# Kernel optimization log

Measured on AMD Instinct MI355X. Metric: run time of the kernel, lower is better.

The kernel has to match this reference:

```python
import jax, jax.numpy as jnp
import numpy as np
import math

NUM_HEADS = 8
KEY_DIM = 32
VALUE_DIM = 32
ERF = 3                      # local window (erf x erf), N = 1 + ERF*ERF key/query positions
PAD = (ERF - 1) // 2
STRIDE = 2
OUT_CH = 256


def unfold_2d(x, k, p, s):
    """Mirror of F.unfold -> (B, k*k, C, Ho, Wo), window index row-major (kh, kw)."""
    B, C, H, W = x.shape
    xp = jnp.pad(x, ((0, 0), (0, 0), (p, p), (p, p)))
    Ho = (H + 2 * p - k) // s + 1
    Wo = (W + 2 * p - k) // s + 1
    pats = [xp[:, :, i:i + s * (Ho - 1) + 1:s, j:j + s * (Wo - 1) + 1:s]
            for i in range(k) for j in range(k)]
    return jnp.stack(pats, axis=1)


def fold_2d(pats, out_hw, k, p, s):
    """Mirror of F.fold (overlap-add inverse of unfold_2d)."""
    B, kk, C, Ho, Wo = pats.shape
    H, W = out_hw
    out = jnp.zeros((B, C, H + 2 * p, W + 2 * p), pats.dtype)
    idx = 0
    for i in range(k):
        for j in range(k):
            out = out.at[:, :, i:i + s * (Ho - 1) + 1:s, j:j + s * (Wo - 1) + 1:s].add(pats[:, idx])
            idx += 1
    return out[:, :, p:p + H, p:p + W]


def setup_inputs() -> dict:
    key = jax.random.key(0)
    ks = jax.random.split(key, 10)
    B = 2
    d = {
        "top_feat": jax.random.normal(ks[0], (B, OUT_CH, 64, 64), jnp.float32),
        "bot_feat": jax.random.normal(ks[1], (B, OUT_CH, 128, 128), jnp.float32),
    }
    qkv_names = ["W_top_key", "W_top_query", "W_top_value", "W_bot_key", "W_bot_query", "W_bot_value"]
    for n, kk in zip(qkv_names, ks[2:8]):
        out_dim = NUM_HEADS * (KEY_DIM if ("key" in n or "query" in n) else VALUE_DIM)
        d[n] = 0.01 * jax.random.normal(kk, (out_dim, OUT_CH), jnp.float32)  # 1x1 conv, no bias
    d["W_top_fuse"] = 0.01 * jax.random.normal(ks[8], (OUT_CH, NUM_HEADS * VALUE_DIM), jnp.float32)
    d["W_bot_fuse"] = 0.01 * jax.random.normal(ks[9], (OUT_CH, NUM_HEADS * VALUE_DIM), jnp.float32)
    return d


def _forward(top_feat, bot_feat, W_top_key, W_top_query, W_top_value,
             W_bot_key, W_bot_query, W_bot_value, W_top_fuse, W_bot_fuse):
    B, _, H, W = top_feat.shape
    Hb, Wb = bot_feat.shape[2], bot_feat.shape[3]

    def proj(x, Wm, dim):  # 1x1 conv then split heads -> (B, h, dim, H', W')
        y = jnp.einsum('oc,bchw->bohw', Wm, x)
        return y.reshape(B, NUM_HEADS, dim, x.shape[2], x.shape[3])

    def unfold_heads(x):  # (B, h, d, Hb, Wb) -> (B, h, e*e, d, H, W)
        d = x.shape[2]
        u = unfold_2d(x.reshape(B * NUM_HEADS, d, Hb, Wb), ERF, PAD, STRIDE)
        return u.reshape(B, NUM_HEADS, ERF * ERF, d, u.shape[3], u.shape[4])

    tK = proj(top_feat, W_top_key, KEY_DIM)[:, :, None]      # (B, h, 1, kd, H, W)
    tQ = proj(top_feat, W_top_query, KEY_DIM)[:, :, None]
    tV = proj(top_feat, W_top_value, VALUE_DIM)[:, :, None]
    bK = unfold_heads(proj(bot_feat, W_bot_key, KEY_DIM))    # (B, h, e*e, kd, H, W)
    bQ = unfold_heads(proj(bot_feat, W_bot_query, KEY_DIM))
    bV = unfold_heads(proj(bot_feat, W_bot_value, VALUE_DIM))

    key_ = jnp.concatenate([tK, bK], axis=2)   # (B, h, N, kd, H, W), N = 1 + e*e
    query = jnp.concatenate([tQ, bQ], axis=2)
    value = jnp.concatenate([tV, bV], axis=2)

    # weight[b,n,k,q,h,w] = <key_k, query_q> / sqrt(kd)   (NOTE: no softmax in original)
    weight = jnp.einsum('bnkdhw,bnqdhw->bnkqhw', key_, query) / math.sqrt(KEY_DIM)
    # out[b,n,q,v,h,w] = sum_k weight[...] * value_k
    out = jnp.einsum('bnkqhw,bnkvhw->bnqvhw', weight, value)  # (B, h, N, vd, H, W)

    top_ret = out[:, :, 0].reshape(B, NUM_HEADS * VALUE_DIM, H, W)
    bot_pat = out[:, :, 1:].reshape(B * NUM_HEADS, ERF * ERF, VALUE_DIM, H, W)
    bot_ret = fold_2d(bot_pat, (Hb, Wb), ERF, PAD, STRIDE).reshape(B, NUM_HEADS * VALUE_DIM, Hb, Wb)

    top_out = jnp.einsum('oc,bchw->bohw', W_top_fuse, top_ret)
    bot_out = jnp.einsum('oc,bchw->bohw', W_bot_fuse, bot_ret)
    return top_out, bot_out


def reference(top_feat, bot_feat, W_top_key, W_top_query, W_top_value,
              W_bot_key, W_bot_query, W_bot_value, W_top_fuse, W_bot_fuse):
    return _forward(top_feat, bot_feat, W_top_key, W_top_query, W_top_value,
                    W_bot_key, W_bot_query, W_bot_value, W_top_fuse, W_bot_fuse)
```

## Files before the change

### kernel.cpp

```cpp
#include <hip/hip_runtime.h>
#include <hip/hip_bf16.h>
#include <math.h>


typedef __attribute__((ext_vector_type(8))) short  bh8;
typedef __attribute__((ext_vector_type(4))) short  bh4;
typedef __attribute__((ext_vector_type(4))) float  f32x4;
typedef unsigned short u16;

static __device__ __forceinline__ u16 f2b(float x) {
    __hip_bfloat16 h = __float2bfloat16(x);
    return __builtin_bit_cast(u16, h);
}
static __device__ __forceinline__ float b2f(u16 u) {
    unsigned v = ((unsigned)u) << 16;
    return __builtin_bit_cast(float, v);
}

static __device__ __forceinline__ void gload16(const u16* g, u16* l) {
    __builtin_amdgcn_global_load_lds(
        (const __attribute__((address_space(1))) unsigned int*)g,
        (__attribute__((address_space(3))) unsigned int*)l, 16, 0, 0);
}

__global__ __launch_bounds__(256) void k_cvt_w(
    const float* w0, const float* w1, const float* w2, const float* w3,
    const float* w4, const float* w5, const float* w6, const float* w7,
    u16* __restrict__ Wb)
{
    const float* srcs[8] = {w0,w1,w2,w3,w4,w5,w6,w7};
    const float* src = srcs[blockIdx.y];
    int i = (blockIdx.x * 256 + threadIdx.x) * 4;
    float4 v = *(const float4*)&src[i];
    u16 tmp[4] = { f2b(v.x), f2b(v.y), f2b(v.z), f2b(v.w) };
    *(uint2*)&Wb[(size_t)blockIdx.y * 65536 + i] = *(uint2*)tmp;
}

__global__ __launch_bounds__(512) void k_proj(
    const float* __restrict__ top_feat, const float* __restrict__ bot_feat,
    const u16* __restrict__ Wb,
    u16* __restrict__ tK, u16* __restrict__ bK, size_t TOPU, size_t BOTU)
{
    const int lbid  = (blockIdx.x & 7) * 120 + (blockIdx.x >> 3);
    const int yb    = lbid / 3;
    const int n0    = (lbid - yb * 3) * 256;
    const bool istop = yb < 64;
    const float* feat = istop ? top_feat : bot_feat;
    const u16* Bw   = istop ? Wb : (Wb + 3 * 65536);
    u16* Yp         = istop ? tK : bK;
    const size_t arrsz = istop ? TOPU : BOTU;
    const int S     = istop ? 4096 : 16384;
    const int m0g   = (istop ? yb : (yb - 64)) * 128;
    const int b     = istop ? (m0g >> 12) : (m0g >> 14);
    const int pix0  = m0g & (S - 1);
    const float* Xb = feat + (size_t)b * 256 * S;
    const int t  = threadIdx.x;
    const int w  = t >> 6, wl = t & 63, l16 = wl & 15, grp = wl >> 4;
    const int wm = w >> 2, wn = w & 3;
    const int apix = t & 127;
    const int oct  = t >> 7;

    __shared__ __align__(16) u16 AT[2][128 * 32];
    __shared__ __align__(16) u16 BT[2][256 * 32];

    float rA[8];

#define PA_LOAD(kk) do {                                                      \
        _Pragma("unroll")                                                     \
        for (int e = 0; e < 8; ++e)                                           \
            rA[e] = Xb[(size_t)((kk) + oct * 8 + e) * S + pix0 + apix];       \
    } while (0)

#define PA_WRITE(bufi) do {                                                   \
        u16 tmp[8];                                                           \
        _Pragma("unroll")                                                     \
        for (int e = 0; e < 8; ++e) tmp[e] = f2b(rA[e]);                      \
        int slot = oct ^ ((apix >> 1) & 3);                                   \
        *(uint4*)&AT[bufi][apix * 32 + slot * 8] = *(uint4*)tmp;              \
    } while (0)

#define PB_STAGE(bufi, kk) do {                                               \
        _Pragma("unroll")                                                     \
        for (int it = 0; it < 2; ++it) {                                      \
            int lin = it * 512 + t;                                           \
            int row = lin >> 2, c = lin & 3;                                  \
            int cs = c ^ ((row >> 1) & 3);                                    \
            gload16(&Bw[(size_t)(n0 + row) * 256 + (kk) + cs * 8],            \
                    &BT[bufi][lin * 8]);                                      \
        }                                                                     \
    } while (0)

    f32x4 acc[4][4];
    #pragma unroll
    for (int i = 0; i < 4; ++i)
        #pragma unroll
        for (int j = 0; j < 4; ++j) acc[i][j] = (f32x4){0.f, 0.f, 0.f, 0.f};

    PA_LOAD(0);
    PB_STAGE(0, 0);
    PA_WRITE(0);
    int cur = 0;
    for (int kt = 0; kt < 8; ++kt) {
        __syncthreads();
        if (kt < 7) {
            PA_LOAD((kt + 1) * 32);
            PB_STAGE(cur ^ 1, (kt + 1) * 32);
        }
        bh8 af[4], bf[4];
        #pragma unroll
        for (int mi = 0; mi < 4; ++mi) {
            int row = wm * 64 + mi * 16 + l16;
            int slot = grp ^ ((row >> 1) & 3);
            af[mi] = *(const bh8*)&AT[cur][row * 32 + slot * 8];
        }
        #pragma unroll
        for (int ni = 0; ni < 4; ++ni) {
            int row = wn * 64 + ni * 16 + l16;
            int slot = grp ^ ((row >> 1) & 3);
            bf[ni] = *(const bh8*)&BT[cur][row * 32 + slot * 8];
        }
        #pragma unroll
        for (int mi = 0; mi < 4; ++mi)
            #pragma unroll
            for (int ni = 0; ni < 4; ++ni)
                acc[mi][ni] = __builtin_amdgcn_mfma_f32_16x16x32_bf16(
                    af[mi], bf[ni], acc[mi][ni], 0, 0, 0);
        if (kt < 7) PA_WRITE(cur ^ 1);
        cur ^= 1;
    }
#undef PA_LOAD
#undef PA_WRITE
#undef PB_STAGE

    #pragma unroll
    for (int mi = 0; mi < 4; ++mi)
        #pragma unroll
        for (int ni = 0; ni < 4; ++ni)
            #pragma unroll
            for (int r = 0; r < 4; ++r) {
                int m = m0g + wm*64 + mi*16 + grp*4 + r;
                int n = n0 + wn*64 + ni*16 + l16;
                Yp[(size_t)(n >> 8) * arrsz + (size_t)m * 256 + (n & 255)]
                    = f2b(acc[mi][ni][r]);
            }
}

#define GEMM_STAGE(bufi, kk) do {                                             \
        _Pragma("unroll")                                                     \
        for (int it = 0; it < 2; ++it) {                                      \
            int lin = it * 256 + t;                                           \
            int row = lin >> 3, c = lin & 7;                                  \
            int cs = c ^ (row & 7);                                           \
            gload16(&A[(size_t)(m0 + row) * 256 + (kk) + cs * 8],             \
                    &AT[bufi][lin * 8]);                                      \
        }                                                                     \
        _Pragma("unroll")                                                     \
        for (int it = 0; it < 8; ++it) {                                      \
            int lin = it * 256 + t;                                           \
            int row = lin >> 3, c = lin & 7;                                  \
            int cs = c ^ (row & 7);                                           \
            gload16(&B[(size_t)(n0 + row) * 256 + (kk) + cs * 8],             \
                    &BT[bufi][lin * 8]);                                      \
        }                                                                     \
    } while (0)

#define GEMM_MAIN()                                                           \
    GEMM_STAGE(0, 0);                                                         \
    int cur = 0;                                                              \
    for (int kt = 0; kt < 4; ++kt) {                                          \
        __syncthreads();                                                      \
        if (kt < 3) GEMM_STAGE(cur ^ 1, (kt + 1) * 64);                       \
        _Pragma("unroll")                                                     \
        for (int ks = 0; ks < 2; ++ks) {                                      \
            bh8 af[4], bf[4];                                                 \
            _Pragma("unroll")                                                 \
            for (int mi = 0; mi < 4; ++mi) {                                  \
                int row = mi * 16 + l16;                                      \
                int pc = (ks * 4 + grp) ^ (row & 7);                          \
                af[mi] = *(const bh8*)&AT[cur][row * 64 + pc * 8];            \
            }                                                                 \
            _Pragma("unroll")                                                 \
            for (int ni = 0; ni < 4; ++ni) {                                  \
                int row = w * 64 + ni * 16 + l16;                             \
                int pc = (ks * 4 + grp) ^ (row & 7);                          \
                bf[ni] = *(const bh8*)&BT[cur][row * 64 + pc * 8];            \
            }                                                                 \
            _Pragma("unroll")                                                 \
            for (int mi = 0; mi < 4; ++mi)                                    \
                _Pragma("unroll")                                             \
                for (int ni = 0; ni < 4; ++ni)                                \
                    acc[mi][ni] = __builtin_amdgcn_mfma_f32_16x16x32_bf16(    \
                        af[mi], bf[ni], acc[mi][ni], 0, 0, 0);                \
        }                                                                     \
        cur ^= 1;                                                             \
    }

__global__ __launch_bounds__(256) void k_fuse(
    const u16* __restrict__ Wb, const u16* __restrict__ tRet,
    const u16* __restrict__ botRet, float* __restrict__ top_out,
    float* __restrict__ bot_out)
{
    const int bid = blockIdx.x;
    const u16* A; const u16* B; float* Yf; int lgS, n0, m0;
    if (bid < 128) {
        A = Wb + 6 * 65536; B = tRet; Yf = top_out; lgS = 12;
        n0 = (bid & 31) * 256; m0 = (bid >> 5) * 64;
    } else {
        int i = bid - 128;
        A = Wb + 7 * 65536; B = botRet; Yf = bot_out; lgS = 14;
        n0 = (i & 127) * 256; m0 = (i >> 7) * 64;
    }
    const int t  = threadIdx.x;
    const int w  = t >> 6, wl = t & 63, l16 = wl & 15, grp = wl >> 4;

    __shared__ __align__(16) u16 AT[2][64 * 64];
    __shared__ __align__(16) u16 BT[2][256 * 64];

    f32x4 acc[4][4];
    #pragma unroll
    for (int i = 0; i < 4; ++i)
        #pragma unroll
        for (int j = 0; j < 4; ++j) acc[i][j] = (f32x4){0.f, 0.f, 0.f, 0.f};

    GEMM_MAIN();

    #pragma unroll
    for (int mi = 0; mi < 4; ++mi)
        #pragma unroll
        for (int ni = 0; ni < 4; ++ni)
            #pragma unroll
            for (int r = 0; r < 4; ++r) {
                int m = m0 + mi*16 + grp*4 + r;
                int n = n0 + w*64 + ni*16 + l16;
                int bb = n >> lgS, s = n & ((1 << lgS) - 1);
                Yf[(((size_t)bb * 256 + m) << lgS) + s] = acc[mi][ni][r];
            }
}

__global__ __launch_bounds__(256) void k_attn(
    const u16* __restrict__ tK, const u16* __restrict__ tQ, const u16* __restrict__ tV,
    const u16* __restrict__ bK, const u16* __restrict__ bQ, const u16* __restrict__ bV,
    u16* __restrict__ tRet, u16* __restrict__ pat)
{
    const int lbid = (blockIdx.x & 7) * 1024 + (blockIdx.x >> 3);
    const int pix = lbid & 4095;
    const int b   = lbid >> 12;
    const int w   = threadIdx.x >> 6;
    const int wl  = threadIdx.x & 63;
    const int l16 = wl & 15, grp = wl >> 4;
    const int y = pix >> 6, x = pix & 63;

    __shared__ u16 Ssm[4][16][24];
    __shared__ __align__(16) u16 Vsm[4][2][16][16];

    const int p = l16;
    bool pvalid = false; int bpix = 0; const bool istop = (p == 0);
    if (p == 0) pvalid = true;
    else if (p < 10) {
        int pm = p - 1; int i = (pm * 11) >> 5; int j = pm - 3 * i;
        int by = 2 * y + i - 1, bx = 2 * x + j - 1;
        pvalid = ((unsigned)by < 128u) && ((unsigned)bx < 128u);
        bpix = by * 128 + bx;
    }
    const size_t topRow = ((size_t)b * 4096  + pix)  * 256;
    const size_t botRow = ((size_t)b * 16384 + bpix) * 256;
    const float scale = 0.17677669529663687f;

    #pragma unroll
    for (int hi = 0; hi < 2; ++hi) {
        const int h = w + hi * 4;
        const size_t off = (istop ? topRow : botRow) + h * 32 + grp * 8;
        bh8 aQ = {}, aK = {}, vV = {};
        if (pvalid) {
            if (istop) {
                aQ = *(const bh8*)(tQ + off);
                aK = *(const bh8*)(tK + off);
                vV = *(const bh8*)(tV + off);
            } else {
                aQ = *(const bh8*)(bQ + off);
                aK = *(const bh8*)(bK + off);
                vV = *(const bh8*)(bV + off);
            }
        }
        *(bh8*)&Vsm[w][grp >> 1][p][(grp & 1) * 8] = vV;

        f32x4 z = {0.f, 0.f, 0.f, 0.f};
        f32x4 sC = __builtin_amdgcn_mfma_f32_16x16x32_bf16(aQ, aK, z, 0, 0, 0);
        #pragma unroll
        for (int r = 0; r < 4; ++r)
            Ssm[w][grp * 4 + r][l16] = f2b(sC[r] * scale);

        bh8 aS = {};
        *(bh4*)&aS = *(const bh4*)&Ssm[w][l16][grp * 4];

        bh8 bv0 = {}, bv1 = {};
        #pragma unroll
        for (int j = 0; j < 4; ++j) {
            bv0[j] = (short)Vsm[w][0][grp * 4 + j][l16];
            bv1[j] = (short)Vsm[w][1][grp * 4 + j][l16];
        }
        f32x4 oc0 = __builtin_amdgcn_mfma_f32_16x16x32_bf16(aS, bv0, z, 0, 0, 0);
        f32x4 oc1 = __builtin_amdgcn_mfma_f32_16x16x32_bf16(aS, bv1, z, 0, 0, 0);

        if (grp == 0) {
            size_t o = topRow + (size_t)h * 32;
            tRet[o + l16]      = f2b(oc0[0]);
            tRet[o + 16 + l16] = f2b(oc1[0]);
        }
        #pragma unroll
        for (int r = 0; r < 4; ++r) {
            int q = grp * 4 + r;
            if (q >= 1 && q <= 9) {
                size_t base = ((((size_t)b * 8 + h) * 9 + (q - 1)) * 4096 + pix) * 32;
                pat[base + l16]      = f2b(oc0[r]);
                pat[base + 16 + l16] = f2b(oc1[r]);
            }
        }
    }
}

__global__ __launch_bounds__(256) void k_fold(
    const u16* __restrict__ pat, u16* __restrict__ botRet)
{
    const int lbid = (blockIdx.x & 7) * 512 + (blockIdx.x >> 3);
    int tid = lbid * 256 + threadIdx.x;
    int vchunk = tid & 3;
    int ri = tid >> 2;
    int b = ri >> 17;
    int bpix = (ri >> 3) & 16383;
    int h = ri & 7;
    int by = bpix >> 7, bx = bpix & 127;
    int v0 = vchunk * 8;

    float acc[8];
    #pragma unroll
    for (int e = 0; e < 8; ++e) acc[e] = 0.f;

    for (int iy = 0; iy < 3; ++iy) {
        int ty = by + 1 - iy;
        if (ty & 1) continue;
        int yy = ty >> 1;
        if ((unsigned)yy >= 64u) continue;
        for (int jx = 0; jx < 3; ++jx) {
            int tx = bx + 1 - jx;
            if (tx & 1) continue;
            int xx = tx >> 1;
            if ((unsigned)xx >= 64u) continue;
            int q = iy * 3 + jx;
            size_t addr = ((((size_t)b * 8 + h) * 9 + q) * 4096 + (yy * 64 + xx)) * 32 + v0;
            uint4 pv = *(const uint4*)&pat[addr];
            const u16* pp = (const u16*)&pv;
            #pragma unroll
            for (int e = 0; e < 8; ++e) acc[e] += b2f(pp[e]);
        }
    }
    u16 tmp[8];
    #pragma unroll
    for (int e = 0; e < 8; ++e) tmp[e] = f2b(acc[e]);
    *(uint4*)&botRet[((size_t)b * 16384 + bpix) * 256 + h * 32 + v0] = *(uint4*)tmp;
}

extern "C" void kernel_launch(void* const* d_in, const int* in_sizes, int n_in,
                              void* d_out, int out_size, void* d_ws, size_t ws_size,
                              hipStream_t stream) {
    const float* top_feat = (const float*)d_in[0];
    const float* bot_feat = (const float*)d_in[1];

    float* out     = (float*)d_out;
    float* top_out = out;
    float* bot_out = out + (size_t)2 * 256 * 4096;

    const size_t TOPU = (size_t)2 * 4096  * 256;
    const size_t BOTU = (size_t)2 * 16384 * 256;
    char* p = (char*)d_ws;
    u16* Wb     = (u16*)p;  p += (size_t)8 * 65536 * 2;
    u16* tK     = (u16*)p;  p += TOPU * 2;
    u16* tQ     = (u16*)p;  p += TOPU * 2;
    u16* tV     = (u16*)p;  p += TOPU * 2;
    u16* bK     = (u16*)p;  p += BOTU * 2;
    u16* bQ     = (u16*)p;  p += BOTU * 2;
    u16* bV     = (u16*)p;  p += BOTU * 2;
    u16* tRet   = (u16*)p;  p += TOPU * 2;
    u16* pat    = (u16*)p;  p += (size_t)2*8*9*4096*32*2;
    u16* botRet = (u16*)p;  p += BOTU * 2;

    k_cvt_w<<<dim3(64, 8), dim3(256), 0, stream>>>(
        (const float*)d_in[2], (const float*)d_in[3], (const float*)d_in[4],
        (const float*)d_in[5], (const float*)d_in[6], (const float*)d_in[7],
        (const float*)d_in[8], (const float*)d_in[9], Wb);

    k_proj<<<dim3(960), dim3(512), 0, stream>>>(top_feat, bot_feat, Wb,
                                                tK, bK, TOPU, BOTU);

    k_attn<<<dim3(8192), dim3(256), 0, stream>>>(tK, tQ, tV, bK, bQ, bV, tRet, pat);

    k_fold<<<dim3(4096), dim3(256), 0, stream>>>(pat, botRet);

    k_fuse<<<dim3(640), dim3(256), 0, stream>>>(Wb, tRet, botRet, top_out, bot_out);
}
```

Baseline: 88.12 us.

## Fuse fold overlap-add into fuse GEMM B-tile staging

Removes the separate k_fold kernel and its botRet intermediate buffer. The bottom-branch fuse GEMM now builds its B tiles directly from the attention patches, summing up to nine neighbour patches in registers before writing to LDS. This saves a kernel launch and a round trip of the botRet buffer through global memory. In exchange, the bottom tiles are loaded with synchronous register loads instead of async global-to-LDS copies, so load latency may be less well overlapped with MFMA work, and each fold is recomputed by every M-block, four times in total.

After: 173.7 us. +97.1%, slower.

```diff
diff --git a/kernel.cpp b/kernel.cpp
--- a/kernel.cpp
+++ b/kernel.cpp
@@ -145,7 +145,31 @@
             }
 }
 
-#define GEMM_STAGE(bufi, kk) do {                                             \
+__global__ __launch_bounds__(256) void k_fuse(
+    const u16* __restrict__ Wb, const u16* __restrict__ tRet,
+    const u16* __restrict__ pat, float* __restrict__ top_out,
+    float* __restrict__ bot_out)
+{
+    const int bid = blockIdx.x;
+    const bool istop = bid < 128;
+    const u16* A; const u16* Bt = nullptr; float* Yf; int lgS, n0, m0;
+    if (istop) {
+        A = Wb + 6 * 65536; Bt = tRet; Yf = top_out; lgS = 12;
+        n0 = (bid & 31) * 256; m0 = (bid >> 5) * 64;
+    } else {
+        int i = bid - 128;
+        A = Wb + 7 * 65536; Yf = bot_out; lgS = 14;
+        n0 = (i & 127) * 256; m0 = (i >> 7) * 64;
+    }
+    const int bb  = n0 >> lgS;
+    const int sp0 = n0 & ((1 << lgS) - 1);
+    const int t  = threadIdx.x;
+    const int w  = t >> 6, wl = t & 63, l16 = wl & 15, grp = wl >> 4;
+
+    __shared__ __align__(16) u16 AT[2][64 * 64];
+    __shared__ __align__(16) u16 BT[2][256 * 64];
+
+#define FA_STAGE(bufi, kk) do {                                               \
         _Pragma("unroll")                                                     \
         for (int it = 0; it < 2; ++it) {                                      \
             int lin = it * 256 + t;                                           \
@@ -154,67 +178,59 @@
             gload16(&A[(size_t)(m0 + row) * 256 + (kk) + cs * 8],             \
                     &AT[bufi][lin * 8]);                                      \
         }                                                                     \
+    } while (0)
+
+#define FB_TOP(bufi, kk) do {                                                 \
         _Pragma("unroll")                                                     \
         for (int it = 0; it < 8; ++it) {                                      \
             int lin = it * 256 + t;                                           \
             int row = lin >> 3, c = lin & 7;                                  \
             int cs = c ^ (row & 7);                                           \
-            gload16(&B[(size_t)(n0 + row) * 256 + (kk) + cs * 8],             \
+            gload16(&Bt[(size_t)(n0 + row) * 256 + (kk) + cs * 8],            \
                     &BT[bufi][lin * 8]);                                      \
         }                                                                     \
     } while (0)
 
-#define GEMM_MAIN()                                                           \
-    GEMM_STAGE(0, 0);                                                         \
-    int cur = 0;                                                              \
-    for (int kt = 0; kt < 4; ++kt) {                                          \
-        __syncthreads();                                                      \
-        if (kt < 3) GEMM_STAGE(cur ^ 1, (kt + 1) * 64);                       \
-        _Pragma("unroll")                                                     \
-        for (int ks = 0; ks < 2; ++ks) {                                      \
-            bh8 af[4], bf[4];                                                 \
+#define FB_BOT(bufi, kk) do {                                                 \
+        _Pragma("unroll")                                                     \
+        for (int it = 0; it < 8; ++it) {                                      \
+            int lin = it * 256 + t;                                           \
+            int row = lin >> 3, c8 = lin & 7;                                 \
+            int cb = (kk) + c8 * 8;                                           \
+            int h = cb >> 5, vv0 = cb & 31;                                   \
+            int bpix = sp0 + row;                                             \
+            int by = bpix >> 7, bx = bpix & 127;                              \
+            float fa[8];                                                      \
             _Pragma("unroll")                                                 \
-            for (int mi = 0; mi < 4; ++mi) {                                  \
-                int row = mi * 16 + l16;                                      \
-                int pc = (ks * 4 + grp) ^ (row & 7);                          \
-                af[mi] = *(const bh8*)&AT[cur][row * 64 + pc * 8];            \
+            for (int e = 0; e < 8; ++e) fa[e] = 0.f;                          \
+            _Pragma("unroll")                                                 \
+            for (int iy = 0; iy < 3; ++iy) {                                  \
+                int ty = by + 1 - iy;                                         \
+                int yy = ty >> 1;                                             \
+                if (!(ty & 1) && (unsigned)yy < 64u) {                        \
+                    _Pragma("unroll")                                         \
+                    for (int jx = 0; jx < 3; ++jx) {                          \
+                        int tx = bx + 1 - jx;                                 \
+                        int xx = tx >> 1;                                     \
+                        if (!(tx & 1) && (unsigned)xx < 64u) {                \
+                            int q = iy * 3 + jx;                              \
+                            size_t ad = ((((size_t)bb * 8 + h) * 9 + q)       \
+                                         * 4096 + (yy * 64 + xx)) * 32 + vv0; \
+                            uint4 pv = *(const uint4*)&pat[ad];               \
+                            const u16* pp = (const u16*)&pv;                  \
+                            _Pragma("unroll")                                 \
+                            for (int e = 0; e < 8; ++e) fa[e] += b2f(pp[e]);  \
+                        }                                                     \
+                    }                                                         \
+                }                                                             \
             }                                                                 \
+            u16 tp[8];                                                        \
             _Pragma("unroll")                                                 \
-            for (int ni = 0; ni < 4; ++ni) {                                  \
-                int row = w * 64 + ni * 16 + l16;                             \
-                int pc = (ks * 4 + grp) ^ (row & 7);                          \
-                bf[ni] = *(const bh8*)&BT[cur][row * 64 + pc * 8];            \
-            }                                                                 \
-            _Pragma("unroll")                                                 \
-            for (int mi = 0; mi < 4; ++mi)                                    \
-                _Pragma("unroll")                                             \
-                for (int ni = 0; ni < 4; ++ni)                                \
-                    acc[mi][ni] = __builtin_amdgcn_mfma_f32_16x16x32_bf16(    \
-                        af[mi], bf[ni], acc[mi][ni], 0, 0, 0);                \
+            for (int e = 0; e < 8; ++e) tp[e] = f2b(fa[e]);                   \
+            int cs = c8 ^ (row & 7);                                          \
+            *(uint4*)&BT[bufi][row * 64 + cs * 8] = *(uint4*)tp;              \
         }                                                                     \
-        cur ^= 1;                                                             \
-    }
-
-__global__ __launch_bounds__(256) void k_fuse(
-    const u16* __restrict__ Wb, const u16* __restrict__ tRet,
-    const u16* __restrict__ botRet, float* __restrict__ top_out,
-    float* __restrict__ bot_out)
-{
-    const int bid = blockIdx.x;
-    const u16* A; const u16* B; float* Yf; int lgS, n0, m0;
-    if (bid < 128) {
-        A = Wb + 6 * 65536; B = tRet; Yf = top_out; lgS = 12;
-        n0 = (bid & 31) * 256; m0 = (bid >> 5) * 64;
-    } else {
-        int i = bid - 128;
-        A = Wb + 7 * 65536; B = botRet; Yf = bot_out; lgS = 14;
-        n0 = (i & 127) * 256; m0 = (i >> 7) * 64;
-    }
-    const int t  = threadIdx.x;
-    const int w  = t >> 6, wl = t & 63, l16 = wl & 15, grp = wl >> 4;
-
-    __shared__ __align__(16) u16 AT[2][64 * 64];
-    __shared__ __align__(16) u16 BT[2][256 * 64];
+    } while (0)
 
     f32x4 acc[4][4];
     #pragma unroll
@@ -222,7 +238,43 @@
         #pragma unroll
         for (int j = 0; j < 4; ++j) acc[i][j] = (f32x4){0.f, 0.f, 0.f, 0.f};
 
-    GEMM_MAIN();
+    FA_STAGE(0, 0);
+    if (istop) FB_TOP(0, 0); else FB_BOT(0, 0);
+    int cur = 0;
+    for (int kt = 0; kt < 4; ++kt) {
+        __syncthreads();
+        if (kt < 3) {
+            FA_STAGE(cur ^ 1, (kt + 1) * 64);
+            if (istop) FB_TOP(cur ^ 1, (kt + 1) * 64);
+            else       FB_BOT(cur ^ 1, (kt + 1) * 64);
+        }
+        #pragma unroll
+        for (int ks = 0; ks < 2; ++ks) {
+            bh8 af[4], bf[4];
+            #pragma unroll
+            for (int mi = 0; mi < 4; ++mi) {
+                int row = mi * 16 + l16;
+                int pc = (ks * 4 + grp) ^ (row & 7);
+                af[mi] = *(const bh8*)&AT[cur][row * 64 + pc * 8];
+            }
+            #pragma unroll
+            for (int ni = 0; ni < 4; ++ni) {
+                int row = w * 64 + ni * 16 + l16;
+                int pc = (ks * 4 + grp) ^ (row & 7);
+                bf[ni] = *(const bh8*)&BT[cur][row * 64 + pc * 8];
+            }
+            #pragma unroll
+            for (int mi = 0; mi < 4; ++mi)
+                #pragma unroll
+                for (int ni = 0; ni < 4; ++ni)
+                    acc[mi][ni] = __builtin_amdgcn_mfma_f32_16x16x32_bf16(
+                        af[mi], bf[ni], acc[mi][ni], 0, 0, 0);
+        }
+        cur ^= 1;
+    }
+#undef FA_STAGE
+#undef FB_TOP
+#undef FB_BOT
 
     #pragma unroll
     for (int mi = 0; mi < 4; ++mi)
@@ -232,7 +284,7 @@
             for (int r = 0; r < 4; ++r) {
                 int m = m0 + mi*16 + grp*4 + r;
                 int n = n0 + w*64 + ni*16 + l16;
-                int bb = n >> lgS, s = n & ((1 << lgS) - 1);
+                int s = n & ((1 << lgS) - 1);
                 Yf[(((size_t)bb * 256 + m) << lgS) + s] = acc[mi][ni][r];
             }
 }
@@ -319,47 +371,6 @@
     }
 }
 
-__global__ __launch_bounds__(256) void k_fold(
-    const u16* __restrict__ pat, u16* __restrict__ botRet)
-{
-    const int lbid = (blockIdx.x & 7) * 512 + (blockIdx.x >> 3);
-    int tid = lbid * 256 + threadIdx.x;
-    int vchunk = tid & 3;
-    int ri = tid >> 2;
-    int b = ri >> 17;
-    int bpix = (ri >> 3) & 16383;
-    int h = ri & 7;
-    int by = bpix >> 7, bx = bpix & 127;
-    int v0 = vchunk * 8;
-
-    float acc[8];
-    #pragma unroll
-    for (int e = 0; e < 8; ++e) acc[e] = 0.f;
-
-    for (int iy = 0; iy < 3; ++iy) {
-        int ty = by + 1 - iy;
-        if (ty & 1) continue;
-        int yy = ty >> 1;
-        if ((unsigned)yy >= 64u) continue;
-        for (int jx = 0; jx < 3; ++jx) {
-            int tx = bx + 1 - jx;
-            if (tx & 1) continue;
-            int xx = tx >> 1;
-            if ((unsigned)xx >= 64u) continue;
-            int q = iy * 3 + jx;
-            size_t addr = ((((size_t)b * 8 + h) * 9 + q) * 4096 + (yy * 64 + xx)) * 32 + v0;
-            uint4 pv = *(const uint4*)&pat[addr];
-            const u16* pp = (const u16*)&pv;
-            #pragma unroll
-            for (int e = 0; e < 8; ++e) acc[e] += b2f(pp[e]);
-        }
-    }
-    u16 tmp[8];
-    #pragma unroll
-    for (int e = 0; e < 8; ++e) tmp[e] = f2b(acc[e]);
-    *(uint4*)&botRet[((size_t)b * 16384 + bpix) * 256 + h * 32 + v0] = *(uint4*)tmp;
-}
-
 extern "C" void kernel_launch(void* const* d_in, const int* in_sizes, int n_in,
                               void* d_out, int out_size, void* d_ws, size_t ws_size,
                               hipStream_t stream) {
@@ -382,7 +393,6 @@
     u16* bV     = (u16*)p;  p += BOTU * 2;
     u16* tRet   = (u16*)p;  p += TOPU * 2;
     u16* pat    = (u16*)p;  p += (size_t)2*8*9*4096*32*2;
-    u16* botRet = (u16*)p;  p += BOTU * 2;
 
     k_cvt_w<<<dim3(64, 8), dim3(256), 0, stream>>>(
         (const float*)d_in[2], (const float*)d_in[3], (const float*)d_in[4],
@@ -394,7 +404,5 @@
 
     k_attn<<<dim3(8192), dim3(256), 0, stream>>>(tK, tQ, tV, bK, bQ, bV, tRet, pat);
 
-    k_fold<<<dim3(4096), dim3(256), 0, stream>>>(pat, botRet);
-
-    k_fuse<<<dim3(640), dim3(256), 0, stream>>>(Wb, tRet, botRet, top_out, bot_out);
-}
+    k_fuse<<<dim3(640), dim3(256), 0, stream>>>(Wb, tRet, pat, top_out, bot_out);
+}
```

## Prefetch two K-tiles ahead in projection GEMM via register double buffering

Applied to the files above, without the earlier changes.

The projection GEMM's main loop is fully unrolled. Global loads for A (fp32 features) and B (bf16 weights) are now issued two K-tiles ahead into alternating register sets, then written to LDS after the MFMA compute. B staging switches from direct global-to-LDS loads to ordinary register loads followed by swizzled LDS stores. The aim is to hide more global memory latency behind compute, at the cost of extra registers, which may lower occupancy.

New measurement: 110.3 us. 1.25x slower.

```diff
diff --git a/kernel.cpp b/kernel.cpp
--- a/kernel.cpp
+++ b/kernel.cpp
@@ -63,30 +63,40 @@
     __shared__ __align__(16) u16 AT[2][128 * 32];
     __shared__ __align__(16) u16 BT[2][256 * 32];
 
-    float rA[8];
-
-#define PA_LOAD(kk) do {                                                      \
+    float a0[8], a1[8];
+    uint4 b0[2], b1[2];
+
+#define PA_LOAD(R, kk) do {                                                   \
         _Pragma("unroll")                                                     \
         for (int e = 0; e < 8; ++e)                                           \
-            rA[e] = Xb[(size_t)((kk) + oct * 8 + e) * S + pix0 + apix];       \
-    } while (0)
-
-#define PA_WRITE(bufi) do {                                                   \
+            R[e] = Xb[(size_t)((kk) + oct * 8 + e) * S + pix0 + apix];        \
+    } while (0)
+
+#define PA_WRITE(bufi, R) do {                                                \
         u16 tmp[8];                                                           \
         _Pragma("unroll")                                                     \
-        for (int e = 0; e < 8; ++e) tmp[e] = f2b(rA[e]);                      \
+        for (int e = 0; e < 8; ++e) tmp[e] = f2b(R[e]);                       \
         int slot = oct ^ ((apix >> 1) & 3);                                   \
         *(uint4*)&AT[bufi][apix * 32 + slot * 8] = *(uint4*)tmp;              \
     } while (0)
 
-#define PB_STAGE(bufi, kk) do {                                               \
+#define PB_LOAD(R, kk) do {                                                   \
         _Pragma("unroll")                                                     \
         for (int it = 0; it < 2; ++it) {                                      \
             int lin = it * 512 + t;                                           \
             int row = lin >> 2, c = lin & 3;                                  \
-            int cs = c ^ ((row >> 1) & 3);                                    \
-            gload16(&Bw[(size_t)(n0 + row) * 256 + (kk) + cs * 8],            \
-                    &BT[bufi][lin * 8]);                                      \
+            R[it] = *(const uint4*)&Bw[(size_t)(n0 + row) * 256               \
+                                       + (kk) + c * 8];                       \
+        }                                                                     \
+    } while (0)
+
+#define PB_WRITE(bufi, R) do {                                                \
+        _Pragma("unroll")                                                     \
+        for (int it = 0; it < 2; ++it) {                                      \
+            int lin = it * 512 + t;                                           \
+            int row = lin >> 2, c = lin & 3;                                  \
+            int slot = c ^ ((row >> 1) & 3);                                  \
+            *(uint4*)&BT[bufi][row * 32 + slot * 8] = R[it];                  \
         }                                                                     \
     } while (0)
 
@@ -96,41 +106,46 @@
         #pragma unroll
         for (int j = 0; j < 4; ++j) acc[i][j] = (f32x4){0.f, 0.f, 0.f, 0.f};
 
-    PA_LOAD(0);
-    PB_STAGE(0, 0);
-    PA_WRITE(0);
-    int cur = 0;
-    for (int kt = 0; kt < 8; ++kt) {
-        __syncthreads();
-        if (kt < 7) {
-            PA_LOAD((kt + 1) * 32);
-            PB_STAGE(cur ^ 1, (kt + 1) * 32);
-        }
-        bh8 af[4], bf[4];
-        #pragma unroll
-        for (int mi = 0; mi < 4; ++mi) {
-            int row = wm * 64 + mi * 16 + l16;
-            int slot = grp ^ ((row >> 1) & 3);
-            af[mi] = *(const bh8*)&AT[cur][row * 32 + slot * 8];
-        }
-        #pragma unroll
-        for (int ni = 0; ni < 4; ++ni) {
-            int row = wn * 64 + ni * 16 + l16;
-            int slot = grp ^ ((row >> 1) & 3);
-            bf[ni] = *(const bh8*)&BT[cur][row * 32 + slot * 8];
-        }
-        #pragma unroll
-        for (int mi = 0; mi < 4; ++mi)
-            #pragma unroll
-            for (int ni = 0; ni < 4; ++ni)
-                acc[mi][ni] = __builtin_amdgcn_mfma_f32_16x16x32_bf16(
-                    af[mi], bf[ni], acc[mi][ni], 0, 0, 0);
-        if (kt < 7) PA_WRITE(cur ^ 1);
-        cur ^= 1;
-    }
+#define PCOMPUTE(CUR) do {                                                    \
+        bh8 af[4], bf[4];                                                     \
+        _Pragma("unroll")                                                     \
+        for (int mi = 0; mi < 4; ++mi) {                                      \
+            int row = wm * 64 + mi * 16 + l16;                                \
+            int slot = grp ^ ((row >> 1) & 3);                                \
+            af[mi] = *(const bh8*)&AT[CUR][row * 32 + slot * 8];              \
+        }                                                                     \
+        _Pragma("unroll")                                                     \
+        for (int ni = 0; ni < 4; ++ni) {                                      \
+            int row = wn * 64 + ni * 16 + l16;                                \
+            int slot = grp ^ ((row >> 1) & 3);                                \
+            bf[ni] = *(const bh8*)&BT[CUR][row * 32 + slot * 8];              \
+        }                                                                     \
+        _Pragma("unroll")                                                     \
+        for (int mi = 0; mi < 4; ++mi)                                        \
+            _Pragma("unroll")                                                 \
+            for (int ni = 0; ni < 4; ++ni)                                    \
+                acc[mi][ni] = __builtin_amdgcn_mfma_f32_16x16x32_bf16(        \
+                    af[mi], bf[ni], acc[mi][ni], 0, 0, 0);                    \
+    } while (0)
+
+    PA_LOAD(a0, 0);   PB_LOAD(b0, 0);
+    PA_LOAD(a1, 32);  PB_LOAD(b1, 32);
+    PA_WRITE(0, a0);  PB_WRITE(0, b0);
+
+    __syncthreads(); PA_LOAD(a0, 64);  PB_LOAD(b0, 64);  PCOMPUTE(0); PA_WRITE(1, a1); PB_WRITE(1, b1);
+    __syncthreads(); PA_LOAD(a1, 96);  PB_LOAD(b1, 96);  PCOMPUTE(1); PA_WRITE(0, a0); PB_WRITE(0, b0);
+    __syncthreads(); PA_LOAD(a0, 128); PB_LOAD(b0, 128); PCOMPUTE(0); PA_WRITE(1, a1); PB_WRITE(1, b1);
+    __syncthreads(); PA_LOAD(a1, 160); PB_LOAD(b1, 160); PCOMPUTE(1); PA_WRITE(0, a0); PB_WRITE(0, b0);
+    __syncthreads(); PA_LOAD(a0, 192); PB_LOAD(b0, 192); PCOMPUTE(0); PA_WRITE(1, a1); PB_WRITE(1, b1);
+    __syncthreads(); PA_LOAD(a1, 224); PB_LOAD(b1, 224); PCOMPUTE(1); PA_WRITE(0, a0); PB_WRITE(0, b0);
+    __syncthreads();                                     PCOMPUTE(0); PA_WRITE(1, a1); PB_WRITE(1, b1);
+    __syncthreads();                                     PCOMPUTE(1);
+
 #undef PA_LOAD
 #undef PA_WRITE
-#undef PB_STAGE
+#undef PB_LOAD
+#undef PB_WRITE
+#undef PCOMPUTE
 
     #pragma unroll
     for (int mi = 0; mi < 4; ++mi)
```
